# Kernel optimization log

Measured on AMD Instinct MI355X. Metric: run time of the kernel, lower is better.

The kernel has to match this reference:

```python
import jax, jax.numpy as jnp
import numpy as np

Y, Z, H, R = 32, 64, 256, 256  # y_dim, z_dim, h_dim, rnn_dim
T, B = 200, 2048


def setup_inputs() -> dict:
    key = jax.random.key(0)
    ks = jax.random.split(key, 32)
    w = lambda k, shape: jax.random.normal(k, shape, jnp.float32) * 0.05
    z32 = lambda n: jnp.zeros((n,), jnp.float32)
    return {
        "states": jax.random.normal(ks[0], (T, B, Y), jnp.float32),
        "eps": jax.random.normal(ks[1], (T - 1, B, Z), jnp.float32),
        # encoder q(z|x,y,h): Linear(2Y+R,H) ReLU Linear(H,H) ReLU
        "enc_w1": w(ks[2], (H, 2 * Y + R)), "enc_b1": z32(H),
        "enc_w2": w(ks[3], (H, H)), "enc_b2": z32(H),
        "enc_mw": w(ks[4], (Z, H)), "enc_mb": z32(Z),
        "enc_sw": w(ks[5], (Z, H)), "enc_sb": z32(Z),
        # prior p(z|y,h): Linear(Y+R,H) ReLU Linear(H,H) ReLU
        "pri_w1": w(ks[6], (H, Y + R)), "pri_b1": z32(H),
        "pri_w2": w(ks[7], (H, H)), "pri_b2": z32(H),
        "pri_mw": w(ks[8], (Z, H)), "pri_mb": z32(Z),
        "pri_sw": w(ks[9], (Z, H)), "pri_sb": z32(Z),
        # decoder p(x|y,z,h): Linear(Y+Z+R,H) ReLU Linear(H,H) ReLU
        "dec_w1": w(ks[10], (H, Y + Z + R)), "dec_b1": z32(H),
        "dec_w2": w(ks[11], (H, H)), "dec_b2": z32(H),
        "dec_mw": w(ks[12], (Y, H)), "dec_mb": z32(Y),
        "dec_sw": w(ks[13], (Y, H)), "dec_sb": z32(Y),
        # GRU(Y+Z -> R), 1 layer; torch gate order [r, z, n]
        "gru_wih": w(ks[14], (3 * R, Y + Z)), "gru_whh": w(ks[15], (3 * R, R)),
        "gru_bih": z32(3 * R), "gru_bhh": z32(3 * R),
    }


def reference(states, eps, enc_w1, enc_b1, enc_w2, enc_b2, enc_mw, enc_mb,
              enc_sw, enc_sb, pri_w1, pri_b1, pri_w2, pri_b2, pri_mw, pri_mb,
              pri_sw, pri_sb, dec_w1, dec_b1, dec_w2, dec_b2, dec_mw, dec_mb,
              dec_sw, dec_sb, gru_wih, gru_whh, gru_bih, gru_bhh):
    batch = states.shape[1]
    rnn_dim = gru_whh.shape[1]
    relu, sp = jax.nn.relu, jax.nn.softplus
    LOG2PI = jnp.float32(np.log(2.0 * np.pi))

    def mlp2(x, w1, b1, w2, b2):
        return relu(relu(x @ w1.T + b1) @ w2.T + b2)

    def step(h, inp):
        y, x, e = inp  # y=states[t], x=states[t+1], e: reparam noise
        enc_h = mlp2(jnp.concatenate([x, y, h], 1), enc_w1, enc_b1, enc_w2, enc_b2)
        em = enc_h @ enc_mw.T + enc_mb
        es = sp(enc_h @ enc_sw.T + enc_sb)
        pri_h = mlp2(jnp.concatenate([y, h], 1), pri_w1, pri_b1, pri_w2, pri_b2)
        pm = pri_h @ pri_mw.T + pri_mb
        ps = sp(pri_h @ pri_sw.T + pri_sb)
        z = em + es * e  # sample_gauss
        dec_h = mlp2(jnp.concatenate([y, z, h], 1), dec_w1, dec_b1, dec_w2, dec_b2)
        dm = dec_h @ dec_mw.T + dec_mb
        ds = sp(dec_h @ dec_sw.T + dec_sb)
        # GRU cell (torch gate order r,z,n)
        gi = jnp.concatenate([x, z], 1) @ gru_wih.T + gru_bih
        gh = h @ gru_whh.T + gru_bhh
        ir, iz, inn = jnp.split(gi, 3, axis=1)
        hr, hz, hn = jnp.split(gh, 3, axis=1)
        r = jax.nn.sigmoid(ir + hr)
        u = jax.nn.sigmoid(iz + hz)
        n = jnp.tanh(inn + r * hn)
        h_new = (1.0 - u) * n + u * h
        kl = 0.5 * jnp.sum(2.0 * jnp.log(ps / es) + (es ** 2 + (em - pm) ** 2) / ps ** 2 - 1.0)
        nll = jnp.sum(jnp.log(ds) + (x - dm) ** 2 / (2.0 * ds ** 2) + 0.5 * LOG2PI)
        return h_new, (kl, nll)

    h0 = jnp.zeros((batch, rnn_dim), states.dtype)
    _, (kls, nlls) = jax.lax.scan(step, h0, (states[:-1], states[1:], eps))
    # out = [kl_loss, recon_loss]
    return jnp.stack([jnp.sum(kls), jnp.sum(nlls)])
```

## Files before the change

kernel.cpp:

```cpp
#include <hip/hip_runtime.h>

typedef unsigned short u16;
typedef unsigned int u32;
typedef __bf16 bf16x8 __attribute__((ext_vector_type(8)));
typedef float f32x4 __attribute__((ext_vector_type(4)));

#define YD 32
#define ZD 64
#define HD 256
#define RD 256
#define TSTEPS 199
#define BB 2048
#define MROWS 16
#define NBLK 128
#define NTHR 1024
#define YS  40
#define ZS  72
#define HS  264
#define HBS 264
#define HES 136
#define HDS 72

enum : int {
  OFF_ENC_W1 = 0,
  OFF_ENC_W2 = 81920,
  OFF_ENC_H  = 147456,
  OFF_PRI_W1 = 180224,
  OFF_PRI_W2 = 253952,
  OFF_PRI_H  = 319488,
  OFF_DEC_W1 = 352256,
  OFF_DEC_W2 = 442368,
  OFF_DEC_H  = 507904,
  OFF_GWIH   = 524288,
  OFF_GWHH   = 598016,
};

__device__ __forceinline__ u16 f2bf(float f) {
  u32 u = __float_as_uint(f);
  u += 0x7fffu + ((u >> 16) & 1u);
  return (u16)(u >> 16);
}
__device__ __forceinline__ float bf2f(u16 b) {
  return __uint_as_float((u32)b << 16);
}
__device__ __forceinline__ float softplus_f(float x) {
  float l = __logf(1.f + __expf(-fabsf(x)));
  return x > 0.f ? x + l : l;
}
__device__ __forceinline__ float sigmoid_f(float x) {
  return __builtin_amdgcn_rcpf(1.f + __expf(-x));
}
__device__ __forceinline__ float tanh_f(float x) {
  float e = __expf(-2.f * fabsf(x));
  float t = (1.f - e) * __builtin_amdgcn_rcpf(1.f + e);
  return x >= 0.f ? t : -t;
}

template<int NT, int RT, int KS, int AS>
__device__ __forceinline__ void gemm_seg(f32x4 (&acc)[NT][RT],
    const u16* __restrict__ W, const int Kw, const int wrow0, const int wk0,
    const u16* A, const int acol0, const int rt0, const int lane)
{
  const int n = lane & 15, quad = lane >> 4;
  bf16x8 b[KS][NT];
  #pragma unroll
  for (int nt = 0; nt < NT; ++nt) {
    const u16* wp = W + (size_t)(wrow0 + nt * 16 + n) * Kw + wk0 + quad * 8;
    #pragma unroll
    for (int ks = 0; ks < KS; ++ks)
      b[ks][nt] = *reinterpret_cast<const bf16x8*>(wp + ks * 32);
  }
  #pragma unroll
  for (int ks = 0; ks < KS; ++ks) {
    bf16x8 a[RT];
    #pragma unroll
    for (int rt = 0; rt < RT; ++rt)
      a[rt] = *reinterpret_cast<const bf16x8*>(A + ((rt0 + rt) * 16 + n) * AS + acol0 + ks * 32 + quad * 8);
    #pragma unroll
    for (int nt = 0; nt < NT; ++nt)
      #pragma unroll
      for (int rt = 0; rt < RT; ++rt)
        acc[nt][rt] = __builtin_amdgcn_mfma_f32_16x16x32_bf16(a[rt], b[ks][nt], acc[nt][rt], 0, 0, 0);
  }
}

template<int NT, int DS>
__device__ __forceinline__ void store_relu_n(const f32x4 (&acc)[NT][1], u16* dst,
    const int col0, const float (&bias)[NT], const int lane)
{
  const int n = lane & 15, quad = lane >> 4;
  #pragma unroll
  for (int nt = 0; nt < NT; ++nt)
    #pragma unroll
    for (int i = 0; i < 4; ++i) {
      float v = fmaxf(acc[nt][0][i] + bias[nt], 0.f);
      dst[(quad * 4 + i) * DS + col0 + nt * 16 + n] = f2bf(v);
    }
}

struct PrepArgs { const float* src[14]; int off[14]; int cnt[14]; };

__global__ void prep_weights(PrepArgs a, u16* __restrict__ dst) {
  const int j = blockIdx.y;
  const float* __restrict__ s = a.src[j];
  u16* d = dst + a.off[j];
  const int nel = a.cnt[j];
  for (int i = blockIdx.x * blockDim.x + threadIdx.x; i < nel; i += gridDim.x * blockDim.x)
    d[i] = f2bf(s[i]);
}

__global__ void zero_out_k(float* out) { if (threadIdx.x < 2) out[threadIdx.x] = 0.f; }

__global__ __launch_bounds__(NTHR, 4)
void vrnn_kernel(const float* __restrict__ states, const float* __restrict__ eps,
                 const float* __restrict__ enc_b1, const float* __restrict__ enc_b2,
                 const float* __restrict__ enc_mb, const float* __restrict__ enc_sb,
                 const float* __restrict__ pri_b1, const float* __restrict__ pri_b2,
                 const float* __restrict__ pri_mb, const float* __restrict__ pri_sb,
                 const float* __restrict__ dec_b1, const float* __restrict__ dec_b2,
                 const float* __restrict__ dec_mb, const float* __restrict__ dec_sb,
                 const float* __restrict__ gbih, const float* __restrict__ gbhh,
                 const u16* __restrict__ ws, float* __restrict__ out)
{
  __shared__ __align__(16) u16 yb[3][MROWS * YS];
  __shared__ __align__(16) u16 zb[2][MROWS * ZS];
  __shared__ __align__(16) u16 hbuf[2][MROWS * HS];
  __shared__ __align__(16) u16 hb1A[MROWS * HBS], hb2A[MROWS * HBS];
  __shared__ __align__(16) u16 hb1P[MROWS * HBS], hb2P[MROWS * HBS];
  __shared__ __align__(16) u16 hb1D[MROWS * HBS], hb2D[MROWS * HBS];
  __shared__ __align__(16) u16 hbhE[2][MROWS * HES];
  __shared__ __align__(16) u16 hbhP[MROWS * HES];
  __shared__ __align__(16) u16 hbhD[MROWS * HDS];

  const int tid = threadIdx.x;
  const int w = tid >> 6, lane = tid & 63;
  const int n = lane & 15, quad = lane >> 4;
  const int r0 = blockIdx.x * MROWS;
  const int n0A = w * 32;

  float b1e[2] = {}, b2e[2] = {}, brg[2] = {}, bug[2] = {}, bing[2] = {}, bhng[2] = {};
  float mbE = 0.f, sbE = 0.f;
  float b1p[4] = {}, b2p[4] = {}, bhP[2] = {};
  float b1d[4] = {}, b2d[4] = {}, bhD = 0.f;
  if (w < 8) {
    #pragma unroll
    for (int s = 0; s < 2; ++s) {
      const int c = n0A + s * 16 + n;
      b1e[s] = enc_b1[c]; b2e[s] = enc_b2[c];
      brg[s] = gbih[c] + gbhh[c];
      bug[s] = gbih[RD + c] + gbhh[RD + c];
      bing[s] = gbih[2 * RD + c];
      bhng[s] = gbhh[2 * RD + c];
    }
    if (w < 4) { mbE = enc_mb[w * 16 + n]; sbE = enc_sb[w * 16 + n]; }
  } else if (w < 12) {
    const int p = w - 8;
    #pragma unroll
    for (int k = 0; k < 4; ++k) {
      const int c = p * 64 + k * 16 + n;
      b1p[k] = pri_b1[c]; b2p[k] = pri_b2[c];
    }
    #pragma unroll
    for (int k = 0; k < 2; ++k) {
      const int r = p * 32 + k * 16 + n;
      bhP[k] = (r < 64) ? pri_mb[r] : pri_sb[r - 64];
    }
  } else {
    const int d_ = w - 12;
    #pragma unroll
    for (int k = 0; k < 4; ++k) {
      const int c = d_ * 64 + k * 16 + n;
      b1d[k] = dec_b1[c]; b2d[k] = dec_b2[c];
    }
    const int r = d_ * 16 + n;
    bhD = (r < 32) ? dec_mb[r] : dec_sb[r - 32];
  }

  for (int i = tid; i < MROWS * (HD / 2); i += NTHR) {
    int row = i >> 7, c = (i & 127) * 2;
    *reinterpret_cast<u32*>(&hbuf[0][row * HS + c]) = 0u;
  }
  if (tid < 256) {
    const int row = tid >> 4, c2 = (tid & 15) * 2;
    float2 a0 = *reinterpret_cast<const float2*>(states + ((size_t)0 * BB + r0 + row) * YD + c2);
    float2 a1 = *reinterpret_cast<const float2*>(states + ((size_t)1 * BB + r0 + row) * YD + c2);
    yb[0][row * YS + c2] = f2bf(a0.x); yb[0][row * YS + c2 + 1] = f2bf(a0.y);
    yb[1][row * YS + c2] = f2bf(a1.x); yb[1][row * YS + c2 + 1] = f2bf(a1.y);
  }
  __syncthreads();

  float hreg[2][4];
  #pragma unroll
  for (int s = 0; s < 2; ++s)
    #pragma unroll
    for (int i = 0; i < 4; ++i) hreg[s][i] = 0.f;

  float kl_acc = 0.f, nll_acc = 0.f;
  int ym0 = 0, ym1 = 1, ym2 = 2;

  for (int t = 0; t <= TSTEPS; ++t) {
    const int pa = t & 1, pb = pa ^ 1;
    f32x4 agh[3][2][1] = {};

    if (w < 8) {
      if (t < TSTEPS) {
        f32x4 acc[2][1] = {};
        gemm_seg<2,1,1,YS>(acc, ws + OFF_ENC_W1, 320, n0A, 0,   yb[ym1], 0, 0, lane);
        gemm_seg<2,1,1,YS>(acc, ws + OFF_ENC_W1, 320, n0A, 32,  yb[ym0], 0, 0, lane);
        gemm_seg<2,1,4,HS>(acc, ws + OFF_ENC_W1, 320, n0A, 64,  hbuf[pa], 0,   0, lane);
        gemm_seg<2,1,4,HS>(acc, ws + OFF_ENC_W1, 320, n0A, 192, hbuf[pa], 128, 0, lane);
        store_relu_n<2, HBS>(acc, hb1A, n0A, b1e, lane);
        gemm_seg<2,1,4,HS>(agh[0], ws + OFF_GWHH, 256, n0A, 0,   hbuf[pa], 0,   0, lane);
        gemm_seg<2,1,4,HS>(agh[0], ws + OFF_GWHH, 256, n0A, 128, hbuf[pa], 128, 0, lane);
      }
    } else if (w < 12) {
      if (t > 0) {
        const int n0 = (w - 8) * 64;
        f32x4 acc[4][1] = {};
        gemm_seg<4,1,1,YS>(acc, ws + OFF_PRI_W1, 288, n0, 0,   yb[ym2], 0, 0, lane);
        gemm_seg<4,1,4,HS>(acc, ws + OFF_PRI_W1, 288, n0, 32,  hbuf[pb], 0,   0, lane);
        gemm_seg<4,1,4,HS>(acc, ws + OFF_PRI_W1, 288, n0, 160, hbuf[pb], 128, 0, lane);
        store_relu_n<4, HBS>(acc, hb1P, n0, b1p, lane);
      }
    } else {
      if (t > 0) {
        const int n0 = (w - 12) * 64;
        f32x4 acc[4][1] = {};
        gemm_seg<4,1,1,YS>(acc, ws + OFF_DEC_W1, 352, n0, 0,   yb[ym2], 0, 0, lane);
        gemm_seg<4,1,2,ZS>(acc, ws + OFF_DEC_W1, 352, n0, 32,  zb[pb], 0, 0, lane);
        gemm_seg<4,1,4,HS>(acc, ws + OFF_DEC_W1, 352, n0, 96,  hbuf[pb], 0,   0, lane);
        gemm_seg<4,1,4,HS>(acc, ws + OFF_DEC_W1, 352, n0, 224, hbuf[pb], 128, 0, lane);
        store_relu_n<4, HBS>(acc, hb1D, n0, b1d, lane);
      }
    }
    __syncthreads();

    if (w < 8) {
      if (t < TSTEPS) {
        f32x4 acc[2][1] = {};
        gemm_seg<2,1,4,HBS>(acc, ws + OFF_ENC_W2, 256, n0A, 0,   hb1A, 0,   0, lane);
        gemm_seg<2,1,4,HBS>(acc, ws + OFF_ENC_W2, 256, n0A, 128, hb1A, 128, 0, lane);
        store_relu_n<2, HBS>(acc, hb2A, n0A, b2e, lane);
        #pragma unroll
        for (int g = 1; g < 3; ++g) {
          gemm_seg<2,1,4,HS>(agh[g], ws + OFF_GWHH, 256, g * RD + n0A, 0,   hbuf[pa], 0,   0, lane);
          gemm_seg<2,1,4,HS>(agh[g], ws + OFF_GWHH, 256, g * RD + n0A, 128, hbuf[pa], 128, 0, lane);
        }
      }
    } else if (w < 12) {
      if (t > 0) {
        const int n0 = (w - 8) * 64;
        f32x4 acc[4][1] = {};
        gemm_seg<4,1,4,HBS>(acc, ws + OFF_PRI_W2, 256, n0, 0,   hb1P, 0,   0, lane);
        gemm_seg<4,1,4,HBS>(acc, ws + OFF_PRI_W2, 256, n0, 128, hb1P, 128, 0, lane);
        store_relu_n<4, HBS>(acc, hb2P, n0, b2p, lane);
      }
    } else {
      if (t > 0) {
        const int n0 = (w - 12) * 64;
        f32x4 acc[4][1] = {};
        gemm_seg<4,1,4,HBS>(acc, ws + OFF_DEC_W2, 256, n0, 0,   hb1D, 0,   0, lane);
        gemm_seg<4,1,4,HBS>(acc, ws + OFF_DEC_W2, 256, n0, 128, hb1D, 128, 0, lane);
        store_relu_n<4, HBS>(acc, hb2D, n0, b2d, lane);
      }
    }
    __syncthreads();

    if (w < 4) {
      if (t < TSTEPS) {
        const int c = w * 16 + n;
        float ev[4];
        #pragma unroll
        for (int i = 0; i < 4; ++i)
          ev[i] = eps[((size_t)t * BB + r0 + quad * 4 + i) * ZD + c];
        f32x4 am[1][1] = {}, asx[1][1] = {};
        gemm_seg<1,1,8,HBS>(am,  ws + OFF_ENC_H, 256, w * 16,      0, hb2A, 0, 0, lane);
        gemm_seg<1,1,8,HBS>(asx, ws + OFF_ENC_H, 256, 64 + w * 16, 0, hb2A, 0, 0, lane);
        u16* he = hbhE[pa];
        #pragma unroll
        for (int i = 0; i < 4; ++i) {
          const int row = quad * 4 + i;
          u16 bm = f2bf(am[0][0][i] + mbE);
          u16 bs = f2bf(softplus_f(asx[0][0][i] + sbE));
          he[row * HES + c] = bm;
          he[row * HES + 64 + c] = bs;
          zb[pa][row * ZS + c] = f2bf(bf2f(bm) + bf2f(bs) * ev[i]);
        }
      }
    } else if (w >= 8 && w < 12) {
      if (t > 0) {
        const int p = w - 8, n0 = p * 32;
        f32x4 acc[2][1] = {};
        gemm_seg<2,1,8,HBS>(acc, ws + OFF_PRI_H, 256, n0, 0, hb2P, 0, 0, lane);
        #pragma unroll
        for (int k = 0; k < 2; ++k)
          #pragma unroll
          for (int i = 0; i < 4; ++i) {
            float v = acc[k][0][i] + bhP[k];
            if (p >= 2) v = softplus_f(v);
            hbhP[(quad * 4 + i) * HES + n0 + k * 16 + n] = f2bf(v);
          }
      }
    } else if (w >= 12) {
      if (t > 0) {
        const int d_ = w - 12;
        f32x4 acc[1][1] = {};
        gemm_seg<1,1,8,HBS>(acc, ws + OFF_DEC_H, 256, d_ * 16, 0, hb2D, 0, 0, lane);
        #pragma unroll
        for (int i = 0; i < 4; ++i) {
          float v = acc[0][0][i] + bhD;
          if (d_ >= 2) v = softplus_f(v);
          hbhD[(quad * 4 + i) * HDS + d_ * 16 + n] = f2bf(v);
        }
      }
    }
    __syncthreads();

    if (w < 8) {
      if (t < TSTEPS) {
        f32x4 agi[3][2][1] = {};
        #pragma unroll
        for (int g = 0; g < 3; ++g) {
          gemm_seg<2,1,1,YS>(agi[g], ws + OFF_GWIH, 96, g * RD + n0A, 0,  yb[ym1], 0, 0, lane);
          gemm_seg<2,1,2,ZS>(agi[g], ws + OFF_GWIH, 96, g * RD + n0A, 32, zb[pa],  0, 0, lane);
        }
        u16* hn = hbuf[pb];
        #pragma unroll
        for (int s = 0; s < 2; ++s)
          #pragma unroll
          for (int i = 0; i < 4; ++i) {
            float r = sigmoid_f(agi[0][s][0][i] + agh[0][s][0][i] + brg[s]);
            float u = sigmoid_f(agi[1][s][0][i] + agh[1][s][0][i] + bug[s]);
            float nn = tanh_f(agi[2][s][0][i] + bing[s] + r * (agh[2][s][0][i] + bhng[s]));
            float hv = (1.f - u) * nn + u * hreg[s][i];
            hreg[s][i] = hv;
            hn[(quad * 4 + i) * HS + n0A + s * 16 + n] = f2bf(hv);
          }
      }
    } else if (w < 12) {
      const int e = tid - 512;
      if (t > 0) {
        const u16* he = hbhE[pb];
        const int m = e >> 4, j0 = e & 15;
        #pragma unroll
        for (int k = 0; k < 4; ++k) {
          const int j = j0 + k * 16;
          float em = bf2f(he[m * HES + j]);
          float es = bf2f(he[m * HES + 64 + j]);
          float pm = bf2f(hbhP[m * HES + j]);
          float ps = bf2f(hbhP[m * HES + 64 + j]);
          float d = em - pm;
          kl_acc += 0.5f * (2.f * __logf(ps * __builtin_amdgcn_rcpf(es))
                            + (es * es + d * d) / (ps * ps) - 1.f);
        }
      }
      if (t + 2 <= TSTEPS) {
        const int row = e >> 4, c2 = (e & 15) * 2;
        float2 v = *reinterpret_cast<const float2*>(states + ((size_t)(t + 2) * BB + r0 + row) * YD + c2);
        u16* dd = &yb[ym2][row * YS + c2];
        dd[0] = f2bf(v.x); dd[1] = f2bf(v.y);
      }
    } else {
      if (t > 0) {
        const int e = tid - 768, m = e >> 4, j2 = (e & 15) * 2;
        float2 xv = *reinterpret_cast<const float2*>(states + ((size_t)t * BB + r0 + m) * YD + j2);
        #pragma unroll
        for (int c = 0; c < 2; ++c) {
          float dm = bf2f(hbhD[m * HDS + j2 + c]);
          float ds = bf2f(hbhD[m * HDS + 32 + j2 + c]);
          float xf = c ? xv.y : xv.x;
          float dd = xf - dm;
          nll_acc += __logf(ds) + dd * dd / (2.f * ds * ds) + 0.91893853320467274178f;
        }
      }
    }
    __syncthreads();

    const int tmp = ym0; ym0 = ym1; ym1 = ym2; ym2 = tmp;
  }

  float kv = kl_acc, nv = nll_acc;
  #pragma unroll
  for (int off = 32; off > 0; off >>= 1) {
    kv += __shfl_down(kv, off, 64);
    nv += __shfl_down(nv, off, 64);
  }
  if (lane == 0) {
    atomicAdd(out + 0, kv);
    atomicAdd(out + 1, nv);
  }
}

extern "C" void kernel_launch(void* const* d_in, const int* in_sizes, int n_in,
                              void* d_out, int out_size, void* d_ws, size_t ws_size,
                              hipStream_t stream) {
  const float* states = (const float*)d_in[0];
  const float* eps    = (const float*)d_in[1];
  u16* ws   = (u16*)d_ws;
  float* out = (float*)d_out;

  PrepArgs pa;
  const int jsrc[14] = {2, 4, 6, 8, 10, 12, 14, 16, 18, 20, 22, 24, 26, 27};
  const int joff[14] = {OFF_ENC_W1, OFF_ENC_W2, OFF_ENC_H, OFF_ENC_H + 16384,
                        OFF_PRI_W1, OFF_PRI_W2, OFF_PRI_H, OFF_PRI_H + 16384,
                        OFF_DEC_W1, OFF_DEC_W2, OFF_DEC_H, OFF_DEC_H + 8192,
                        OFF_GWIH, OFF_GWHH};
  const int jcnt[14] = {81920, 65536, 16384, 16384,
                        73728, 65536, 16384, 16384,
                        90112, 65536, 8192, 8192,
                        73728, 196608};
  for (int j = 0; j < 14; ++j) {
    pa.src[j] = (const float*)d_in[jsrc[j]];
    pa.off[j] = joff[j];
    pa.cnt[j] = jcnt[j];
  }

  zero_out_k<<<dim3(1), dim3(64), 0, stream>>>(out);
  prep_weights<<<dim3(64, 14), dim3(256), 0, stream>>>(pa, ws);
  vrnn_kernel<<<dim3(NBLK), dim3(NTHR), 0, stream>>>(
      states, eps,
      (const float*)d_in[3],  (const float*)d_in[5],
      (const float*)d_in[7],  (const float*)d_in[9],
      (const float*)d_in[11], (const float*)d_in[13],
      (const float*)d_in[15], (const float*)d_in[17],
      (const float*)d_in[19], (const float*)d_in[21],
      (const float*)d_in[23], (const float*)d_in[25],
      (const float*)d_in[28], (const float*)d_in[29],
      ws, out);
}
```

Measured before the change: 10.08 ms.

## Halve block to 8 waves with wider per-wave tiles and pipelined weight loads

Shrinks each block from 16 to 8 wavefronts, giving each wave twice as many output columns in the encoder, prior and decoder GEMMs. Weight fragment loads are split from the MFMA loops and staged with sched_barriers, so the next weight chunk is fetched while the current one is being multiplied. The GRU input-gate work is reordered gate by gate to keep register pressure down, and the head work is redistributed. This trades fewer waves for hiding latency against more per-wave work and more registers, under launch bounds of 2 blocks per CU.

```diff
diff --git a/kernel.cpp b/kernel.cpp
--- a/kernel.cpp
+++ b/kernel.cpp
@@ -13,13 +13,15 @@
 #define BB 2048
 #define MROWS 16
 #define NBLK 128
-#define NTHR 1024
+#define NTHR 512
 #define YS  40
 #define ZS  72
 #define HS  264
 #define HBS 264
 #define HES 136
 #define HDS 72
+
+#define SB0() __builtin_amdgcn_sched_barrier(0)
 
 enum : int {
   OFF_ENC_W1 = 0,
@@ -56,31 +58,32 @@
   return x >= 0.f ? t : -t;
 }
 
-template<int NT, int RT, int KS, int AS>
-__device__ __forceinline__ void gemm_seg(f32x4 (&acc)[NT][RT],
-    const u16* __restrict__ W, const int Kw, const int wrow0, const int wk0,
-    const u16* A, const int acol0, const int rt0, const int lane)
-{
+template<int NT, int KS>
+struct WF { bf16x8 b[KS][NT]; };
+
+template<int NT, int KS>
+__device__ __forceinline__ void wload(WF<NT, KS>& f, const u16* __restrict__ W,
+    const int Kw, const int wrow0, const int wk0, const int lane) {
   const int n = lane & 15, quad = lane >> 4;
-  bf16x8 b[KS][NT];
   #pragma unroll
   for (int nt = 0; nt < NT; ++nt) {
     const u16* wp = W + (size_t)(wrow0 + nt * 16 + n) * Kw + wk0 + quad * 8;
     #pragma unroll
     for (int ks = 0; ks < KS; ++ks)
-      b[ks][nt] = *reinterpret_cast<const bf16x8*>(wp + ks * 32);
-  }
+      f.b[ks][nt] = *reinterpret_cast<const bf16x8*>(wp + ks * 32);
+  }
+}
+
+template<int NT, int KS, int AS>
+__device__ __forceinline__ void gemm_b(f32x4 (&acc)[NT][1], const WF<NT, KS>& f,
+    const u16* A, const int acol0, const int lane) {
+  const int n = lane & 15, quad = lane >> 4;
   #pragma unroll
   for (int ks = 0; ks < KS; ++ks) {
-    bf16x8 a[RT];
-    #pragma unroll
-    for (int rt = 0; rt < RT; ++rt)
-      a[rt] = *reinterpret_cast<const bf16x8*>(A + ((rt0 + rt) * 16 + n) * AS + acol0 + ks * 32 + quad * 8);
+    bf16x8 a = *reinterpret_cast<const bf16x8*>(A + n * AS + acol0 + ks * 32 + quad * 8);
     #pragma unroll
     for (int nt = 0; nt < NT; ++nt)
-      #pragma unroll
-      for (int rt = 0; rt < RT; ++rt)
-        acc[nt][rt] = __builtin_amdgcn_mfma_f32_16x16x32_bf16(a[rt], b[ks][nt], acc[nt][rt], 0, 0, 0);
+      acc[nt][0] = __builtin_amdgcn_mfma_f32_16x16x32_bf16(a, f.b[ks][nt], acc[nt][0], 0, 0, 0);
   }
 }
 
@@ -111,7 +114,7 @@
 
 __global__ void zero_out_k(float* out) { if (threadIdx.x < 2) out[threadIdx.x] = 0.f; }
 
-__global__ __launch_bounds__(NTHR, 4)
+__global__ __launch_bounds__(NTHR, 2)
 void vrnn_kernel(const float* __restrict__ states, const float* __restrict__ eps,
                  const float* __restrict__ enc_b1, const float* __restrict__ enc_b2,
                  const float* __restrict__ enc_mb, const float* __restrict__ enc_sb,
@@ -136,15 +139,27 @@
   const int w = tid >> 6, lane = tid & 63;
   const int n = lane & 15, quad = lane >> 4;
   const int r0 = blockIdx.x * MROWS;
-  const int n0A = w * 32;
-
-  float b1e[2] = {}, b2e[2] = {}, brg[2] = {}, bug[2] = {}, bing[2] = {}, bhng[2] = {};
-  float mbE = 0.f, sbE = 0.f;
-  float b1p[4] = {}, b2p[4] = {}, bhP[2] = {};
-  float b1d[4] = {}, b2d[4] = {}, bhD = 0.f;
-  if (w < 8) {
-    #pragma unroll
-    for (int s = 0; s < 2; ++s) {
+  const int n0A = w * 64;
+  const int n0B = (w & 1) * 128;
+
+  const u16* __restrict__ wE1 = ws + OFF_ENC_W1;
+  const u16* __restrict__ wE2 = ws + OFF_ENC_W2;
+  const u16* __restrict__ wEH = ws + OFF_ENC_H;
+  const u16* __restrict__ wP1 = ws + OFF_PRI_W1;
+  const u16* __restrict__ wP2 = ws + OFF_PRI_W2;
+  const u16* __restrict__ wPH = ws + OFF_PRI_H;
+  const u16* __restrict__ wD1 = ws + OFF_DEC_W1;
+  const u16* __restrict__ wD2 = ws + OFF_DEC_W2;
+  const u16* __restrict__ wDH = ws + OFF_DEC_H;
+  const u16* __restrict__ wGI = ws + OFF_GWIH;
+  const u16* __restrict__ wGH = ws + OFF_GWHH;
+
+  float b1e[4] = {}, b2e[4] = {}, brg[4] = {}, bug[4] = {}, bing[4] = {}, bhng[4] = {};
+  float b1p[8] = {}, b2p[8] = {}, mbE2[2] = {}, sbE2[2] = {}, bhPm[2] = {}, bhPs[2] = {};
+  float b1d[8] = {}, b2d[8] = {}, bhDm = 0.f, bhDs = 0.f;
+  if (w < 4) {
+    #pragma unroll
+    for (int s = 0; s < 4; ++s) {
       const int c = n0A + s * 16 + n;
       b1e[s] = enc_b1[c]; b2e[s] = enc_b2[c];
       brg[s] = gbih[c] + gbhh[c];
@@ -152,28 +167,27 @@
       bing[s] = gbih[2 * RD + c];
       bhng[s] = gbhh[2 * RD + c];
     }
-    if (w < 4) { mbE = enc_mb[w * 16 + n]; sbE = enc_sb[w * 16 + n]; }
-  } else if (w < 12) {
-    const int p = w - 8;
-    #pragma unroll
-    for (int k = 0; k < 4; ++k) {
-      const int c = p * 64 + k * 16 + n;
+  } else if (w < 6) {
+    const int p = w - 4;
+    #pragma unroll
+    for (int k = 0; k < 8; ++k) {
+      const int c = n0B + k * 16 + n;
       b1p[k] = pri_b1[c]; b2p[k] = pri_b2[c];
     }
     #pragma unroll
-    for (int k = 0; k < 2; ++k) {
-      const int r = p * 32 + k * 16 + n;
-      bhP[k] = (r < 64) ? pri_mb[r] : pri_sb[r - 64];
+    for (int s = 0; s < 2; ++s) {
+      const int d = p * 32 + s * 16 + n;
+      mbE2[s] = enc_mb[d]; sbE2[s] = enc_sb[d];
+      bhPm[s] = pri_mb[d]; bhPs[s] = pri_sb[d];
     }
   } else {
-    const int d_ = w - 12;
-    #pragma unroll
-    for (int k = 0; k < 4; ++k) {
-      const int c = d_ * 64 + k * 16 + n;
+    const int q = w - 6;
+    #pragma unroll
+    for (int k = 0; k < 8; ++k) {
+      const int c = n0B + k * 16 + n;
       b1d[k] = dec_b1[c]; b2d[k] = dec_b2[c];
     }
-    const int r = d_ * 16 + n;
-    bhD = (r < 32) ? dec_mb[r] : dec_sb[r - 32];
+    bhDm = dec_mb[q * 16 + n]; bhDs = dec_sb[q * 16 + n];
   }
 
   for (int i = tid; i < MROWS * (HD / 2); i += NTHR) {
@@ -189,9 +203,9 @@
   }
   __syncthreads();
 
-  float hreg[2][4];
+  float hreg[4][4];
   #pragma unroll
-  for (int s = 0; s < 2; ++s)
+  for (int s = 0; s < 4; ++s)
     #pragma unroll
     for (int i = 0; i < 4; ++i) hreg[s][i] = 0.f;
 
@@ -200,151 +214,255 @@
 
   for (int t = 0; t <= TSTEPS; ++t) {
     const int pa = t & 1, pb = pa ^ 1;
-    f32x4 agh[3][2][1] = {};
-
-    if (w < 8) {
-      if (t < TSTEPS) {
-        f32x4 acc[2][1] = {};
-        gemm_seg<2,1,1,YS>(acc, ws + OFF_ENC_W1, 320, n0A, 0,   yb[ym1], 0, 0, lane);
-        gemm_seg<2,1,1,YS>(acc, ws + OFF_ENC_W1, 320, n0A, 32,  yb[ym0], 0, 0, lane);
-        gemm_seg<2,1,4,HS>(acc, ws + OFF_ENC_W1, 320, n0A, 64,  hbuf[pa], 0,   0, lane);
-        gemm_seg<2,1,4,HS>(acc, ws + OFF_ENC_W1, 320, n0A, 192, hbuf[pa], 128, 0, lane);
-        store_relu_n<2, HBS>(acc, hb1A, n0A, b1e, lane);
-        gemm_seg<2,1,4,HS>(agh[0], ws + OFF_GWHH, 256, n0A, 0,   hbuf[pa], 0,   0, lane);
-        gemm_seg<2,1,4,HS>(agh[0], ws + OFF_GWHH, 256, n0A, 128, hbuf[pa], 128, 0, lane);
-      }
-    } else if (w < 12) {
-      if (t > 0) {
-        const int n0 = (w - 8) * 64;
-        f32x4 acc[4][1] = {};
-        gemm_seg<4,1,1,YS>(acc, ws + OFF_PRI_W1, 288, n0, 0,   yb[ym2], 0, 0, lane);
-        gemm_seg<4,1,4,HS>(acc, ws + OFF_PRI_W1, 288, n0, 32,  hbuf[pb], 0,   0, lane);
-        gemm_seg<4,1,4,HS>(acc, ws + OFF_PRI_W1, 288, n0, 160, hbuf[pb], 128, 0, lane);
-        store_relu_n<4, HBS>(acc, hb1P, n0, b1p, lane);
-      }
-    } else {
-      if (t > 0) {
-        const int n0 = (w - 12) * 64;
-        f32x4 acc[4][1] = {};
-        gemm_seg<4,1,1,YS>(acc, ws + OFF_DEC_W1, 352, n0, 0,   yb[ym2], 0, 0, lane);
-        gemm_seg<4,1,2,ZS>(acc, ws + OFF_DEC_W1, 352, n0, 32,  zb[pb], 0, 0, lane);
-        gemm_seg<4,1,4,HS>(acc, ws + OFF_DEC_W1, 352, n0, 96,  hbuf[pb], 0,   0, lane);
-        gemm_seg<4,1,4,HS>(acc, ws + OFF_DEC_W1, 352, n0, 224, hbuf[pb], 128, 0, lane);
-        store_relu_n<4, HBS>(acc, hb1D, n0, b1d, lane);
-      }
-    }
-    __syncthreads();
-
-    if (w < 8) {
-      if (t < TSTEPS) {
-        f32x4 acc[2][1] = {};
-        gemm_seg<2,1,4,HBS>(acc, ws + OFF_ENC_W2, 256, n0A, 0,   hb1A, 0,   0, lane);
-        gemm_seg<2,1,4,HBS>(acc, ws + OFF_ENC_W2, 256, n0A, 128, hb1A, 128, 0, lane);
-        store_relu_n<2, HBS>(acc, hb2A, n0A, b2e, lane);
-        #pragma unroll
-        for (int g = 1; g < 3; ++g) {
-          gemm_seg<2,1,4,HS>(agh[g], ws + OFF_GWHH, 256, g * RD + n0A, 0,   hbuf[pa], 0,   0, lane);
-          gemm_seg<2,1,4,HS>(agh[g], ws + OFF_GWHH, 256, g * RD + n0A, 128, hbuf[pa], 128, 0, lane);
-        }
-      }
-    } else if (w < 12) {
-      if (t > 0) {
-        const int n0 = (w - 8) * 64;
-        f32x4 acc[4][1] = {};
-        gemm_seg<4,1,4,HBS>(acc, ws + OFF_PRI_W2, 256, n0, 0,   hb1P, 0,   0, lane);
-        gemm_seg<4,1,4,HBS>(acc, ws + OFF_PRI_W2, 256, n0, 128, hb1P, 128, 0, lane);
-        store_relu_n<4, HBS>(acc, hb2P, n0, b2p, lane);
-      }
-    } else {
-      if (t > 0) {
-        const int n0 = (w - 12) * 64;
-        f32x4 acc[4][1] = {};
-        gemm_seg<4,1,4,HBS>(acc, ws + OFF_DEC_W2, 256, n0, 0,   hb1D, 0,   0, lane);
-        gemm_seg<4,1,4,HBS>(acc, ws + OFF_DEC_W2, 256, n0, 128, hb1D, 128, 0, lane);
-        store_relu_n<4, HBS>(acc, hb2D, n0, b2d, lane);
-      }
-    }
-    __syncthreads();
+    f32x4 agh[3][4][1] = {};
 
     if (w < 4) {
       if (t < TSTEPS) {
-        const int c = w * 16 + n;
-        float ev[4];
+        WF<4,1> fx, fy; WF<4,4> fh0, fh1, fg0, fg1;
+        wload(fx, wE1, 320, n0A, 0, lane);
+        wload(fy, wE1, 320, n0A, 32, lane); SB0();
+        wload(fh0, wE1, 320, n0A, 64, lane); SB0();
+        f32x4 acc[4][1] = {};
+        gemm_b<4,1,YS>(acc, fx, yb[ym1], 0, lane);
+        gemm_b<4,1,YS>(acc, fy, yb[ym0], 0, lane); SB0();
+        wload(fh1, wE1, 320, n0A, 192, lane); SB0();
+        gemm_b<4,4,HS>(acc, fh0, hbuf[pa], 0, lane); SB0();
+        wload(fg0, wGH, 256, n0A, 0, lane); SB0();
+        gemm_b<4,4,HS>(acc, fh1, hbuf[pa], 128, lane); SB0();
+        wload(fg1, wGH, 256, n0A, 128, lane); SB0();
+        store_relu_n<4, HBS>(acc, hb1A, n0A, b1e, lane);
+        gemm_b<4,4,HS>(agh[0], fg0, hbuf[pa], 0, lane); SB0();
+        gemm_b<4,4,HS>(agh[0], fg1, hbuf[pa], 128, lane);
+      }
+    } else if (w < 6) {
+      if (t > 0) {
+        WF<8,1> py; WF<8,2> ph0, ph1, ph2, ph3;
+        wload(py, wP1, 288, n0B, 0, lane);
+        wload(ph0, wP1, 288, n0B, 32, lane); SB0();
+        wload(ph1, wP1, 288, n0B, 96, lane); SB0();
+        f32x4 acc[8][1] = {};
+        gemm_b<8,1,YS>(acc, py, yb[ym2], 0, lane);
+        gemm_b<8,2,HS>(acc, ph0, hbuf[pb], 0, lane); SB0();
+        wload(ph2, wP1, 288, n0B, 160, lane); SB0();
+        gemm_b<8,2,HS>(acc, ph1, hbuf[pb], 64, lane); SB0();
+        wload(ph3, wP1, 288, n0B, 224, lane); SB0();
+        gemm_b<8,2,HS>(acc, ph2, hbuf[pb], 128, lane);
+        gemm_b<8,2,HS>(acc, ph3, hbuf[pb], 192, lane);
+        store_relu_n<8, HBS>(acc, hb1P, n0B, b1p, lane);
+      }
+    } else {
+      if (t > 0) {
+        WF<8,1> dy; WF<8,2> dz, dh0, dh1, dh2, dh3;
+        wload(dy, wD1, 352, n0B, 0, lane);
+        wload(dz, wD1, 352, n0B, 32, lane); SB0();
+        wload(dh0, wD1, 352, n0B, 96, lane); SB0();
+        f32x4 acc[8][1] = {};
+        gemm_b<8,1,YS>(acc, dy, yb[ym2], 0, lane);
+        gemm_b<8,2,ZS>(acc, dz, zb[pb], 0, lane); SB0();
+        wload(dh1, wD1, 352, n0B, 160, lane); SB0();
+        gemm_b<8,2,HS>(acc, dh0, hbuf[pb], 0, lane); SB0();
+        wload(dh2, wD1, 352, n0B, 224, lane); SB0();
+        gemm_b<8,2,HS>(acc, dh1, hbuf[pb], 64, lane); SB0();
+        wload(dh3, wD1, 352, n0B, 288, lane); SB0();
+        gemm_b<8,2,HS>(acc, dh2, hbuf[pb], 128, lane);
+        gemm_b<8,2,HS>(acc, dh3, hbuf[pb], 192, lane);
+        store_relu_n<8, HBS>(acc, hb1D, n0B, b1d, lane);
+      }
+    }
+    __syncthreads();
+
+    if (w < 4) {
+      if (t < TSTEPS) {
+        WF<4,4> e2a, e2b, g1a, g1b;
+        wload(e2a, wE2, 256, n0A, 0, lane); SB0();
+        wload(e2b, wE2, 256, n0A, 128, lane); SB0();
+        f32x4 acc[4][1] = {};
+        gemm_b<4,4,HBS>(acc, e2a, hb1A, 0, lane); SB0();
+        wload(g1a, wGH, 256, RD + n0A, 0, lane); SB0();
+        gemm_b<4,4,HBS>(acc, e2b, hb1A, 128, lane); SB0();
+        wload(g1b, wGH, 256, RD + n0A, 128, lane); SB0();
+        store_relu_n<4, HBS>(acc, hb2A, n0A, b2e, lane);
+        gemm_b<4,4,HS>(agh[1], g1a, hbuf[pa], 0, lane); SB0();
+        gemm_b<4,4,HS>(agh[1], g1b, hbuf[pa], 128, lane);
+      }
+    } else if (w < 6) {
+      if (t > 0) {
+        WF<8,2> q0, q1, q2, q3;
+        wload(q0, wP2, 256, n0B, 0, lane); SB0();
+        wload(q1, wP2, 256, n0B, 64, lane); SB0();
+        f32x4 acc[8][1] = {};
+        gemm_b<8,2,HBS>(acc, q0, hb1P, 0, lane); SB0();
+        wload(q2, wP2, 256, n0B, 128, lane); SB0();
+        gemm_b<8,2,HBS>(acc, q1, hb1P, 64, lane); SB0();
+        wload(q3, wP2, 256, n0B, 192, lane); SB0();
+        gemm_b<8,2,HBS>(acc, q2, hb1P, 128, lane);
+        gemm_b<8,2,HBS>(acc, q3, hb1P, 192, lane);
+        store_relu_n<8, HBS>(acc, hb2P, n0B, b2p, lane);
+      }
+    } else {
+      if (t > 0) {
+        WF<8,2> q0, q1, q2, q3;
+        wload(q0, wD2, 256, n0B, 0, lane); SB0();
+        wload(q1, wD2, 256, n0B, 64, lane); SB0();
+        f32x4 acc[8][1] = {};
+        gemm_b<8,2,HBS>(acc, q0, hb1D, 0, lane); SB0();
+        wload(q2, wD2, 256, n0B, 128, lane); SB0();
+        gemm_b<8,2,HBS>(acc, q1, hb1D, 64, lane); SB0();
+        wload(q3, wD2, 256, n0B, 192, lane); SB0();
+        gemm_b<8,2,HBS>(acc, q2, hb1D, 128, lane);
+        gemm_b<8,2,HBS>(acc, q3, hb1D, 192, lane);
+        store_relu_n<8, HBS>(acc, hb2D, n0B, b2d, lane);
+      }
+    }
+    __syncthreads();
+
+    if (w < 4) {
+      if (t < TSTEPS) {
+        WF<4,4> g2a, g2b;
+        wload(g2a, wGH, 256, 2 * RD + n0A, 0, lane); SB0();
+        wload(g2b, wGH, 256, 2 * RD + n0A, 128, lane); SB0();
+        gemm_b<4,4,HS>(agh[2], g2a, hbuf[pa], 0, lane); SB0();
+        gemm_b<4,4,HS>(agh[2], g2b, hbuf[pa], 128, lane);
+      }
+    } else if (w < 6) {
+      const int p = w - 4;
+      if (t < TSTEPS) {
+        float ev[2][4];
         #pragma unroll
-        for (int i = 0; i < 4; ++i)
-          ev[i] = eps[((size_t)t * BB + r0 + quad * 4 + i) * ZD + c];
-        f32x4 am[1][1] = {}, asx[1][1] = {};
-        gemm_seg<1,1,8,HBS>(am,  ws + OFF_ENC_H, 256, w * 16,      0, hb2A, 0, 0, lane);
-        gemm_seg<1,1,8,HBS>(asx, ws + OFF_ENC_H, 256, 64 + w * 16, 0, hb2A, 0, 0, lane);
+        for (int s = 0; s < 2; ++s)
+          #pragma unroll
+          for (int i = 0; i < 4; ++i)
+            ev[s][i] = eps[((size_t)t * BB + r0 + quad * 4 + i) * ZD + p * 32 + s * 16 + n];
+        WF<2,4> ema, emb, esa, esb;
+        wload(ema, wEH, 256, p * 32, 0, lane);
+        wload(emb, wEH, 256, p * 32, 128, lane); SB0();
+        wload(esa, wEH, 256, 64 + p * 32, 0, lane);
+        wload(esb, wEH, 256, 64 + p * 32, 128, lane); SB0();
+        f32x4 aem[2][1] = {}, aes[2][1] = {};
+        gemm_b<2,4,HBS>(aem, ema, hb2A, 0, lane);
+        gemm_b<2,4,HBS>(aem, emb, hb2A, 128, lane);
+        gemm_b<2,4,HBS>(aes, esa, hb2A, 0, lane);
+        gemm_b<2,4,HBS>(aes, esb, hb2A, 128, lane);
         u16* he = hbhE[pa];
-        #pragma unroll
-        for (int i = 0; i < 4; ++i) {
-          const int row = quad * 4 + i;
-          u16 bm = f2bf(am[0][0][i] + mbE);
-          u16 bs = f2bf(softplus_f(asx[0][0][i] + sbE));
-          he[row * HES + c] = bm;
-          he[row * HES + 64 + c] = bs;
-          zb[pa][row * ZS + c] = f2bf(bf2f(bm) + bf2f(bs) * ev[i]);
-        }
-      }
-    } else if (w >= 8 && w < 12) {
-      if (t > 0) {
-        const int p = w - 8, n0 = p * 32;
-        f32x4 acc[2][1] = {};
-        gemm_seg<2,1,8,HBS>(acc, ws + OFF_PRI_H, 256, n0, 0, hb2P, 0, 0, lane);
-        #pragma unroll
-        for (int k = 0; k < 2; ++k)
-          #pragma unroll
-          for (int i = 0; i < 4; ++i) {
-            float v = acc[k][0][i] + bhP[k];
-            if (p >= 2) v = softplus_f(v);
-            hbhP[(quad * 4 + i) * HES + n0 + k * 16 + n] = f2bf(v);
-          }
-      }
-    } else if (w >= 12) {
-      if (t > 0) {
-        const int d_ = w - 12;
-        f32x4 acc[1][1] = {};
-        gemm_seg<1,1,8,HBS>(acc, ws + OFF_DEC_H, 256, d_ * 16, 0, hb2D, 0, 0, lane);
-        #pragma unroll
-        for (int i = 0; i < 4; ++i) {
-          float v = acc[0][0][i] + bhD;
-          if (d_ >= 2) v = softplus_f(v);
-          hbhD[(quad * 4 + i) * HDS + d_ * 16 + n] = f2bf(v);
-        }
-      }
-    }
-    __syncthreads();
-
-    if (w < 8) {
-      if (t < TSTEPS) {
-        f32x4 agi[3][2][1] = {};
-        #pragma unroll
-        for (int g = 0; g < 3; ++g) {
-          gemm_seg<2,1,1,YS>(agi[g], ws + OFF_GWIH, 96, g * RD + n0A, 0,  yb[ym1], 0, 0, lane);
-          gemm_seg<2,1,2,ZS>(agi[g], ws + OFF_GWIH, 96, g * RD + n0A, 32, zb[pa],  0, 0, lane);
-        }
-        u16* hn = hbuf[pb];
         #pragma unroll
         for (int s = 0; s < 2; ++s)
           #pragma unroll
           for (int i = 0; i < 4; ++i) {
-            float r = sigmoid_f(agi[0][s][0][i] + agh[0][s][0][i] + brg[s]);
-            float u = sigmoid_f(agi[1][s][0][i] + agh[1][s][0][i] + bug[s]);
-            float nn = tanh_f(agi[2][s][0][i] + bing[s] + r * (agh[2][s][0][i] + bhng[s]));
-            float hv = (1.f - u) * nn + u * hreg[s][i];
-            hreg[s][i] = hv;
-            hn[(quad * 4 + i) * HS + n0A + s * 16 + n] = f2bf(hv);
+            const int row = quad * 4 + i, d = p * 32 + s * 16 + n;
+            u16 bm = f2bf(aem[s][0][i] + mbE2[s]);
+            u16 bs = f2bf(softplus_f(aes[s][0][i] + sbE2[s]));
+            he[row * HES + d] = bm;
+            he[row * HES + 64 + d] = bs;
+            zb[pa][row * ZS + d] = f2bf(bf2f(bm) + bf2f(bs) * ev[s][i]);
           }
       }
-    } else if (w < 12) {
-      const int e = tid - 512;
+      if (t > 0) {
+        WF<2,4> pma, pmb, psa, psb;
+        wload(pma, wPH, 256, p * 32, 0, lane);
+        wload(pmb, wPH, 256, p * 32, 128, lane); SB0();
+        wload(psa, wPH, 256, 64 + p * 32, 0, lane);
+        wload(psb, wPH, 256, 64 + p * 32, 128, lane); SB0();
+        f32x4 apm[2][1] = {}, aps[2][1] = {};
+        gemm_b<2,4,HBS>(apm, pma, hb2P, 0, lane);
+        gemm_b<2,4,HBS>(apm, pmb, hb2P, 128, lane);
+        gemm_b<2,4,HBS>(aps, psa, hb2P, 0, lane);
+        gemm_b<2,4,HBS>(aps, psb, hb2P, 128, lane);
+        #pragma unroll
+        for (int s = 0; s < 2; ++s)
+          #pragma unroll
+          for (int i = 0; i < 4; ++i) {
+            const int row = quad * 4 + i, d = p * 32 + s * 16 + n;
+            hbhP[row * HES + d] = f2bf(apm[s][0][i] + bhPm[s]);
+            hbhP[row * HES + 64 + d] = f2bf(softplus_f(aps[s][0][i] + bhPs[s]));
+          }
+      }
+    } else {
+      if (t > 0) {
+        const int q = w - 6;
+        WF<1,4> m0, m1, s0, s1;
+        wload(m0, wDH, 256, q * 16, 0, lane);
+        wload(m1, wDH, 256, q * 16, 128, lane); SB0();
+        wload(s0, wDH, 256, 32 + q * 16, 0, lane);
+        wload(s1, wDH, 256, 32 + q * 16, 128, lane); SB0();
+        f32x4 adm[1][1] = {}, ads[1][1] = {};
+        gemm_b<1,4,HBS>(adm, m0, hb2D, 0, lane);
+        gemm_b<1,4,HBS>(adm, m1, hb2D, 128, lane);
+        gemm_b<1,4,HBS>(ads, s0, hb2D, 0, lane);
+        gemm_b<1,4,HBS>(ads, s1, hb2D, 128, lane);
+        #pragma unroll
+        for (int i = 0; i < 4; ++i) {
+          const int row = quad * 4 + i;
+          hbhD[row * HDS + q * 16 + n] = f2bf(adm[0][0][i] + bhDm);
+          hbhD[row * HDS + 32 + q * 16 + n] = f2bf(softplus_f(ads[0][0][i] + bhDs));
+        }
+      }
+    }
+    __syncthreads();
+
+    if (w < 4) {
+      if (t < TSTEPS) {
+        WF<4,1> rx, ux, nx; WF<4,2> rz, uz, nz;
+        wload(rx, wGI, 96, n0A, 0, lane);
+        wload(rz, wGI, 96, n0A, 32, lane); SB0();
+        wload(ux, wGI, 96, RD + n0A, 0, lane);
+        wload(uz, wGI, 96, RD + n0A, 32, lane); SB0();
+        {
+          f32x4 agi[4][1] = {};
+          gemm_b<4,1,YS>(agi, rx, yb[ym1], 0, lane);
+          gemm_b<4,2,ZS>(agi, rz, zb[pa], 0, lane);
+          #pragma unroll
+          for (int s = 0; s < 4; ++s)
+            #pragma unroll
+            for (int i = 0; i < 4; ++i) {
+              float r = sigmoid_f(agi[s][0][i] + agh[0][s][0][i] + brg[s]);
+              agh[2][s][0][i] = r * (agh[2][s][0][i] + bhng[s]);
+            }
+        }
+        SB0();
+        wload(nx, wGI, 96, 2 * RD + n0A, 0, lane);
+        wload(nz, wGI, 96, 2 * RD + n0A, 32, lane); SB0();
+        {
+          f32x4 agi[4][1] = {};
+          gemm_b<4,1,YS>(agi, ux, yb[ym1], 0, lane);
+          gemm_b<4,2,ZS>(agi, uz, zb[pa], 0, lane);
+          #pragma unroll
+          for (int s = 0; s < 4; ++s)
+            #pragma unroll
+            for (int i = 0; i < 4; ++i)
+              agh[1][s][0][i] = sigmoid_f(agi[s][0][i] + agh[1][s][0][i] + bug[s]);
+        }
+        SB0();
+        {
+          f32x4 agi[4][1] = {};
+          gemm_b<4,1,YS>(agi, nx, yb[ym1], 0, lane);
+          gemm_b<4,2,ZS>(agi, nz, zb[pa], 0, lane);
+          u16* hn = hbuf[pb];
+          #pragma unroll
+          for (int s = 0; s < 4; ++s)
+            #pragma unroll
+            for (int i = 0; i < 4; ++i) {
+              float nn = tanh_f(agi[s][0][i] + bing[s] + agh[2][s][0][i]);
+              float u = agh[1][s][0][i];
+              float hv = (1.f - u) * nn + u * hreg[s][i];
+              hreg[s][i] = hv;
+              hn[(quad * 4 + i) * HS + n0A + s * 16 + n] = f2bf(hv);
+            }
+        }
+      }
+    } else if (w < 6) {
+      const int e = (w - 4) * 64 + lane;
+      if (t + 2 <= TSTEPS) {
+        const int row = e >> 3, c4 = (e & 7) * 4;
+        float4 v = *reinterpret_cast<const float4*>(states + ((size_t)(t + 2) * BB + r0 + row) * YD + c4);
+        u16* dd = &yb[ym2][row * YS + c4];
+        dd[0] = f2bf(v.x); dd[1] = f2bf(v.y); dd[2] = f2bf(v.z); dd[3] = f2bf(v.w);
+      }
       if (t > 0) {
         const u16* he = hbhE[pb];
-        const int m = e >> 4, j0 = e & 15;
+        const int m = e >> 3, j0 = (e & 7) * 8;
         #pragma unroll
-        for (int k = 0; k < 4; ++k) {
-          const int j = j0 + k * 16;
+        for (int k = 0; k < 8; ++k) {
+          const int j = j0 + k;
           float em = bf2f(he[m * HES + j]);
           float es = bf2f(he[m * HES + 64 + j]);
           float pm = bf2f(hbhP[m * HES + j]);
@@ -354,21 +472,15 @@
                             + (es * es + d * d) / (ps * ps) - 1.f);
         }
       }
-      if (t + 2 <= TSTEPS) {
-        const int row = e >> 4, c2 = (e & 15) * 2;
-        float2 v = *reinterpret_cast<const float2*>(states + ((size_t)(t + 2) * BB + r0 + row) * YD + c2);
-        u16* dd = &yb[ym2][row * YS + c2];
-        dd[0] = f2bf(v.x); dd[1] = f2bf(v.y);
-      }
     } else {
       if (t > 0) {
-        const int e = tid - 768, m = e >> 4, j2 = (e & 15) * 2;
-        float2 xv = *reinterpret_cast<const float2*>(states + ((size_t)t * BB + r0 + m) * YD + j2);
+        const int e = (w - 6) * 64 + lane, m = e >> 3, j = (e & 7) * 4;
+        float4 xv = *reinterpret_cast<const float4*>(states + ((size_t)t * BB + r0 + m) * YD + j);
         #pragma unroll
-        for (int c = 0; c < 2; ++c) {
-          float dm = bf2f(hbhD[m * HDS + j2 + c]);
-          float ds = bf2f(hbhD[m * HDS + 32 + j2 + c]);
-          float xf = c ? xv.y : xv.x;
+        for (int c = 0; c < 4; ++c) {
+          float dm = bf2f(hbhD[m * HDS + j + c]);
+          float ds = bf2f(hbhD[m * HDS + 32 + j + c]);
+          float xf = (c == 0) ? xv.x : (c == 1) ? xv.y : (c == 2) ? xv.z : xv.w;
           float dd = xf - dm;
           nll_acc += __logf(ds) + dd * dd / (2.f * ds * ds) + 0.91893853320467274178f;
         }
```

Result: slower. 14.79 ms (+46.7%).
